# Kernel optimization log

Hardware: AMD Instinct MI355X
Metric: run time of the kernel (lower is better)

## Reference

```python
import jax, jax.numpy as jnp
import numpy as np

B, S = 4, 2048
D_MODEL, N_HEADS, D_KV = 1024, 16, 64
NUM_BUCKETS, MAX_DIST = 32, 128


def _relative_position_bucket(relative_position, num_buckets=NUM_BUCKETS, max_distance=MAX_DIST):
    # bidirectional (encoder) variant, faithful to FlaxT5Attention._relative_position_bucket
    num_buckets = num_buckets // 2
    relative_buckets = (relative_position > 0).astype(jnp.int32) * num_buckets
    rp = jnp.abs(relative_position)
    max_exact = num_buckets // 2
    is_small = rp < max_exact
    rp_large = max_exact + (
        jnp.log(rp.astype(jnp.float32) / max_exact)
        / np.log(max_distance / max_exact)
        * (num_buckets - max_exact)
    )
    rp_large = jnp.minimum(rp_large, num_buckets - 1)
    return relative_buckets + jnp.where(is_small, rp, rp_large.astype(jnp.int32))


def setup_inputs() -> dict:
    key = jax.random.key(0)
    ks = jax.random.split(key, 6)
    return {
        "hidden_states": jax.random.normal(ks[0], (B, S, D_MODEL), jnp.float32),
        "mask": jnp.zeros((B, S), jnp.float32),  # additive mask, 0 = attend
        "wq": jax.random.normal(ks[1], (D_MODEL, N_HEADS * D_KV), jnp.float32) * 0.02,
        "wk": jax.random.normal(ks[2], (D_MODEL, N_HEADS * D_KV), jnp.float32) * 0.02,
        "wv": jax.random.normal(ks[3], (D_MODEL, N_HEADS * D_KV), jnp.float32) * 0.02,
        "wo": jax.random.normal(ks[4], (N_HEADS * D_KV, D_MODEL), jnp.float32) * 0.02,
        "rel_bias": jax.random.normal(ks[5], (NUM_BUCKETS, N_HEADS), jnp.float32) * 0.02,
    }


def reference(hidden_states, mask, wq, wk, wv, wo, rel_bias):
    b, s, _ = hidden_states.shape
    # QKV projections, split heads -> [B, S, H, D]
    q = (hidden_states @ wq).reshape(b, s, N_HEADS, D_KV)
    k = (hidden_states @ wk).reshape(b, s, N_HEADS, D_KV)
    v = (hidden_states @ wv).reshape(b, s, N_HEADS, D_KV)

    # relative position bias -> [1, H, S, S]
    pos = jnp.arange(s, dtype=jnp.int32)
    relative_position = pos[None, :] - pos[:, None]  # memory - query
    buckets = _relative_position_bucket(relative_position)
    position_bias = rel_bias[buckets].transpose(2, 0, 1)[None]  # [1,H,S,S]
    # encoder path: additive mask expanded to [B,1,1,K]
    position_bias = position_bias + mask[:, None, None, :]

    # flax dot_product_attention_weights scales q by 1/sqrt(depth)
    scores = jnp.einsum("bqhd,bkhd->bhqk", q / jnp.sqrt(jnp.float32(D_KV)), k)
    attn_weights = jax.nn.softmax(scores + position_bias, axis=-1)

    attn_output = jnp.einsum("bhqk,bkhd->bqhd", attn_weights, v)
    attn_output = attn_output.reshape(b, s, N_HEADS * D_KV) @ wo
    return attn_output, position_bias
```

## Files before the change

kernel.cpp:

```cpp
#include <hip/hip_runtime.h>
#include <hip/hip_bf16.h>

typedef __attribute__((ext_vector_type(8))) short bf16x8;
typedef __attribute__((ext_vector_type(8))) unsigned short u16x8;
typedef __attribute__((ext_vector_type(4))) float f32x4;

#define B_   4
#define S_   2048
#define H_   16
#define DKV  64
#define DM   1024

static __device__ __forceinline__ f32x4 mfma16(bf16x8 a, bf16x8 b, f32x4 c){
  return __builtin_amdgcn_mfma_f32_16x16x32_bf16(a, b, c, 0, 0, 0);
}
static __device__ __forceinline__ void gload_lds16(const void* g, void* l){
  __builtin_amdgcn_global_load_lds((const __attribute__((address_space(1))) void*)g,
                                   (__attribute__((address_space(3))) void*)l, 16, 0, 0);
}
static __device__ __forceinline__ unsigned short f2b(float f){
  union { __hip_bfloat16 b; unsigned short u; } x;
  x.b = __float2bfloat16(f);
  return x.u;
}

__global__ void cast_h_kernel(const float* __restrict__ in, unsigned short* __restrict__ out, int n4){
  int i = blockIdx.x * 256 + threadIdx.x;
  if (i >= n4) return;
  float4 v = reinterpret_cast<const float4*>(in)[i];
  ushort4 r;
  r.x = f2b(v.x); r.y = f2b(v.y); r.z = f2b(v.z); r.w = f2b(v.w);
  reinterpret_cast<ushort4*>(out)[i] = r;
}

__global__ void transpose_w_kernel(const float* __restrict__ w0, const float* __restrict__ w1,
                                   const float* __restrict__ w2, const float* __restrict__ w3,
                                   unsigned short* o0, unsigned short* o1,
                                   unsigned short* o2, unsigned short* o3){
  int z = blockIdx.z;
  const float* src = (z==0) ? w0 : (z==1) ? w1 : (z==2) ? w2 : w3;
  unsigned short* dst = (z==0) ? o0 : (z==1) ? o1 : (z==2) ? o2 : o3;
  __shared__ float tile[32][33];
  int bx = blockIdx.x * 32, by = blockIdx.y * 32;
  int tx = threadIdx.x, ty = threadIdx.y;
  #pragma unroll
  for (int i = 0; i < 32; i += 8)
    tile[ty + i][tx] = src[(size_t)(by + ty + i) * DM + bx + tx];
  __syncthreads();
  #pragma unroll
  for (int i = 0; i < 32; i += 8)
    dst[(size_t)(bx + ty + i) * DM + by + tx] = f2b(tile[tx][ty + i]);
}

__global__ void build_table_kernel(const float* __restrict__ rel_bias, float* __restrict__ table_t){
  int i = blockIdx.x * 256 + threadIdx.x;
  if (i >= 16 * 4095) return;
  int h = i / 4095;
  int idx = i - h * 4095;
  int rel = idx - 2047;
  int bucket = (rel > 0) ? 16 : 0;
  int rp = (rel < 0) ? -rel : rel;
  int off;
  if (rp < 8) off = rp;
  else off = 8 + (rp>=12) + (rp>=16) + (rp>=23) + (rp>=32) + (rp>=46) + (rp>=64) + (rp>=91);
  table_t[i] = rel_bias[(bucket + off) * 16 + h];
}

__global__ void posbias_kernel(const float* __restrict__ relb, const float* __restrict__ mask,
                               float* __restrict__ out){
  __shared__ float rbh[32];
  int row = blockIdx.x;
  int q = row & (S_ - 1);
  int h = (row >> 11) & (H_ - 1);
  int b = row >> 15;
  int tid = threadIdx.x;
  if (tid < 32) rbh[tid] = relb[tid * 16 + h];
  __syncthreads();
  const float* mrow = mask + b * S_;
  float* orow = out + (size_t)row * S_;
  int k0 = tid * 8;
  #pragma unroll
  for (int c = 0; c < 2; ++c){
    float4 mv = *(const float4*)(mrow + k0 + c * 4);
    float4 v;
    #pragma unroll
    for (int j = 0; j < 4; ++j){
      int k = k0 + c * 4 + j;
      int rel = k - q;
      int bucket = (rel > 0) ? 16 : 0;
      int rp = (rel < 0) ? -rel : rel;
      int off = (rp < 8) ? rp
              : 8 + (rp>=12) + (rp>=16) + (rp>=23) + (rp>=32) + (rp>=46) + (rp>=64) + (rp>=91);
      (&v.x)[j] = rbh[bucket + off] + (&mv.x)[j];
    }
    *(float4*)(orow + k0 + c*4) = v;
  }
}

template<int MODE>
__global__ __launch_bounds__(256, 2) void gemm_bt_kernel(
    const unsigned short* __restrict__ A, const unsigned short* __restrict__ Bt,
    void* __restrict__ outp, int M, int N, int K, float scale)
{
  __shared__ __align__(16) unsigned short As[2][128 * 32];
  __shared__ __align__(16) unsigned short Bs[2][128 * 32];
  int tid = threadIdx.x; int lane = tid & 63; int w = tid >> 6;
  int wr = w >> 1, wc = w & 1;
  int n0 = blockIdx.x * 128, m0 = blockIdx.y * 128;
  const char* Ab = (const char*)A;
  const char* Bb = (const char*)Bt;
  size_t Kb = (size_t)K * 2;

  f32x4 acc[4][4];
  #pragma unroll
  for (int i = 0; i < 4; ++i)
    #pragma unroll
    for (int j = 0; j < 4; ++j) acc[i][j] = (f32x4){0.f, 0.f, 0.f, 0.f};

  auto stage = [&](int kt, int bsel){
    size_t k0b = (size_t)kt * 64;
    #pragma unroll
    for (int c = 0; c < 2; ++c){
      int o = c * 4096 + w * 1024 + lane * 16;
      int row = o >> 6;
      int wbl = (o & 63) ^ (((row >> 1) & 3) << 4);
      gload_lds16(Ab + (size_t)(m0 + row) * Kb + k0b + wbl, (char*)As[bsel] + c * 4096 + w * 1024);
      gload_lds16(Bb + (size_t)(n0 + row) * Kb + k0b + wbl, (char*)Bs[bsel] + c * 4096 + w * 1024);
    }
  };

  int nk = K >> 5;
  int buf = 0;
  stage(0, 0);
  for (int kt = 0; kt < nk; ++kt){
    __syncthreads();
    if (kt + 1 < nk) stage(kt + 1, buf ^ 1);
    bf16x8 af[4], bfr[4];
    #pragma unroll
    for (int f = 0; f < 4; ++f){
      int row = wr * 64 + f * 16 + (lane & 15);
      int byt = (row * 64 + ((lane >> 4) * 16)) ^ (((row >> 1) & 3) << 4);
      af[f] = *(const bf16x8*)((const char*)As[buf] + byt);
    }
    #pragma unroll
    for (int f = 0; f < 4; ++f){
      int row = wc * 64 + f * 16 + (lane & 15);
      int byt = (row * 64 + ((lane >> 4) * 16)) ^ (((row >> 1) & 3) << 4);
      bfr[f] = *(const bf16x8*)((const char*)Bs[buf] + byt);
    }
    #pragma unroll
    for (int i = 0; i < 4; ++i)
      #pragma unroll
      for (int j = 0; j < 4; ++j)
        acc[i][j] = mfma16(af[i], bfr[j], acc[i][j]);
    buf ^= 1;
  }

  #pragma unroll
  for (int i = 0; i < 4; ++i){
    #pragma unroll
    for (int j = 0; j < 4; ++j){
      #pragma unroll
      for (int r = 0; r < 4; ++r){
        int m = m0 + wr * 64 + i * 16 + ((lane >> 4) * 4) + r;
        int n = n0 + wc * 64 + j * 16 + (lane & 15);
        if (MODE == 0){
          ((float*)outp)[(size_t)m * N + n] = acc[i][j][r] * scale;
        } else {
          int sel = n >> 10, nn = n & 1023;
          float v = acc[i][j][r] * (sel == 0 ? 0.125f : 1.0f);
          int b = m >> 11, s = m & 2047, hh = nn >> 6, d = nn & 63;
          ((unsigned short*)outp)[(size_t)sel * 8388608 +
              (((size_t)(b * H_ + hh) * S_) + s) * DKV + d] = f2b(v);
        }
      }
    }
  }
}

__global__ __launch_bounds__(256, 2) void attn_mfma_kernel(
    const unsigned short* __restrict__ Qp, const unsigned short* __restrict__ Kp,
    const unsigned short* __restrict__ Vp, const float* __restrict__ table_t,
    const float* __restrict__ mask, unsigned short* __restrict__ outp)
{
  __shared__ __align__(16) unsigned short Ks[64][72];
  __shared__ __align__(16) unsigned short Vs[64][72];
  __shared__ __align__(16) unsigned short Ps[4][32][72];
  __shared__ float bias_s[191];
  __shared__ float mask_s[64];

  int bid = blockIdx.x;
  int qt = bid & 15; int h = (bid >> 4) & 15; int b = bid >> 8;
  int qb = qt * 128;
  const unsigned short* qptr = Qp + ((size_t)(b * H_ + h) * S_ + qb) * DKV;
  const unsigned short* kptr = Kp + (size_t)(b * H_ + h) * S_ * DKV;
  const unsigned short* vptr = Vp + (size_t)(b * H_ + h) * S_ * DKV;
  int tid = threadIdx.x; int lane = tid & 63; int w = tid >> 6;

  bf16x8 qf[2][2];
  #pragma unroll
  for (int qs = 0; qs < 2; ++qs){
    const unsigned short* qrow = qptr + (size_t)(w * 32 + qs * 16 + (lane & 15)) * DKV + 8 * (lane >> 4);
    qf[qs][0] = *(const bf16x8*)qrow;
    qf[qs][1] = *(const bf16x8*)(qrow + 32);
  }
  float l_r[2][4] = {{0.f,0.f,0.f,0.f},{0.f,0.f,0.f,0.f}};
  f32x4 o_acc[2][4];
  #pragma unroll
  for (int qs = 0; qs < 2; ++qs)
    #pragma unroll
    for (int d = 0; d < 4; ++d) o_acc[qs][d] = (f32x4){0.f, 0.f, 0.f, 0.f};

  int bias_base = h * 4095 + (2047 - qb - 127);

  int skey = tid & 63;
  int sd0  = (tid >> 6) * 16;

  u16x8 ka, kb2, va, vb2;
  float biasr = 0.f, maskr = 0.f;
  auto gload = [&](int k0){
    const unsigned short* krow = kptr + (size_t)(k0 + skey) * DKV + sd0;
    const unsigned short* vrow = vptr + (size_t)(k0 + skey) * DKV + sd0;
    ka  = *(const u16x8*)krow;
    kb2 = *(const u16x8*)(krow + 8);
    va  = *(const u16x8*)vrow;
    vb2 = *(const u16x8*)(vrow + 8);
    if (tid < 191) biasr = table_t[bias_base + k0 + tid];
    else if (tid >= 192) maskr = mask[b * S_ + k0 + (tid - 192)];
  };
  auto lwrite = [&](){
    *(u16x8*)&Ks[skey][sd0]     = ka;
    *(u16x8*)&Ks[skey][sd0 + 8] = kb2;
    #pragma unroll
    for (int j = 0; j < 8; ++j){
      Vs[sd0 + j][skey]     = va[j];
      Vs[sd0 + 8 + j][skey] = vb2[j];
    }
    if (tid < 191) bias_s[tid] = biasr;
    else if (tid >= 192) mask_s[tid - 192] = maskr;
  };

  gload(0);
  lwrite();
  for (int k0 = 0; k0 < S_; k0 += 64){
    __syncthreads();
    if (k0 + 64 < S_) gload(k0 + 64);

    bf16x8 kf[4][2];
    #pragma unroll
    for (int kb = 0; kb < 4; ++kb)
      #pragma unroll
      for (int ks = 0; ks < 2; ++ks)
        kf[kb][ks] = *(const bf16x8*)&Ks[kb * 16 + (lane & 15)][ks * 32 + (lane >> 4) * 8];

    float t[2][4][4];
    float rs[2][4] = {{0.f,0.f,0.f,0.f},{0.f,0.f,0.f,0.f}};
    #pragma unroll
    for (int qs = 0; qs < 2; ++qs){
      f32x4 sc[4];
      #pragma unroll
      for (int kb = 0; kb < 4; ++kb){
        sc[kb] = (f32x4){0.f, 0.f, 0.f, 0.f};
        #pragma unroll
        for (int ks = 0; ks < 2; ++ks)
          sc[kb] = mfma16(qf[qs][ks], kf[kb][ks], sc[kb]);
      }
      #pragma unroll
      for (int kb = 0; kb < 4; ++kb){
        int k_l = kb * 16 + (lane & 15);
        float mk = mask_s[k_l];
        #pragma unroll
        for (int r = 0; r < 4; ++r){
          int q_l = w * 32 + qs * 16 + (lane >> 4) * 4 + r;
          float p = __expf(sc[kb][r] + bias_s[k_l - q_l + 127] + mk);
          t[qs][kb][r] = p;
          rs[qs][r] += p;
        }
      }
    }
    #pragma unroll
    for (int qs = 0; qs < 2; ++qs)
      #pragma unroll
      for (int r = 0; r < 4; ++r){
        #pragma unroll
        for (int off = 1; off < 16; off <<= 1)
          rs[qs][r] += __shfl_xor(rs[qs][r], off, 64);
        l_r[qs][r] += rs[qs][r];
      }
    #pragma unroll
    for (int qs = 0; qs < 2; ++qs)
      #pragma unroll
      for (int kb = 0; kb < 4; ++kb)
        #pragma unroll
        for (int r = 0; r < 4; ++r)
          Ps[w][qs * 16 + (lane >> 4) * 4 + r][kb * 16 + (lane & 15)] = f2b(t[qs][kb][r]);

    bf16x8 vf[4][2];
    #pragma unroll
    for (int db = 0; db < 4; ++db)
      #pragma unroll
      for (int ks = 0; ks < 2; ++ks)
        vf[db][ks] = *(const bf16x8*)&Vs[db * 16 + (lane & 15)][ks * 32 + (lane >> 4) * 8];
    #pragma unroll
    for (int qs = 0; qs < 2; ++qs){
      bf16x8 pa[2];
      #pragma unroll
      for (int ks = 0; ks < 2; ++ks)
        pa[ks] = *(const bf16x8*)&Ps[w][qs * 16 + (lane & 15)][ks * 32 + (lane >> 4) * 8];
      #pragma unroll
      for (int db = 0; db < 4; ++db)
        #pragma unroll
        for (int ks = 0; ks < 2; ++ks)
          o_acc[qs][db] = mfma16(pa[ks], vf[db][ks], o_acc[qs][db]);
    }

    __syncthreads();
    if (k0 + 64 < S_) lwrite();
  }

  #pragma unroll
  for (int qs = 0; qs < 2; ++qs)
    #pragma unroll
    for (int r = 0; r < 4; ++r){
      float inv = 1.0f / l_r[qs][r];
      int qg = qb + w * 32 + qs * 16 + (lane >> 4) * 4 + r;
      size_t rowoff = ((size_t)b * S_ + qg) * DM + h * DKV;
      #pragma unroll
      for (int db = 0; db < 4; ++db)
        outp[rowoff + db * 16 + (lane & 15)] = f2b(o_acc[qs][db][r] * inv);
    }
}

extern "C" void kernel_launch(void* const* d_in, const int* in_sizes, int n_in,
                              void* d_out, int out_size, void* d_ws, size_t ws_size,
                              hipStream_t stream) {
  const float* hs   = (const float*)d_in[0];
  const float* msk  = (const float*)d_in[1];
  const float* wq   = (const float*)d_in[2];
  const float* wk   = (const float*)d_in[3];
  const float* wv   = (const float*)d_in[4];
  const float* wo   = (const float*)d_in[5];
  const float* relb = (const float*)d_in[6];

  float* out_attn = (float*)d_out;
  float* out_pb   = (float*)d_out + (size_t)B_ * S_ * DM;

  const size_t SCRATCH_NEED = 76021760;
  char* ws = (ws_size >= SCRATCH_NEED && d_ws) ? (char*)d_ws : (char*)out_pb;

  unsigned short* h_bf  = (unsigned short*)(ws + 0);
  unsigned short* wqkv_t= (unsigned short*)(ws + 16777216);
  unsigned short* wk_t  = (unsigned short*)(ws + 18874368);
  unsigned short* wv_t  = (unsigned short*)(ws + 20971520);
  unsigned short* wo_t  = (unsigned short*)(ws + 23068672);
  unsigned short* qkv_b = (unsigned short*)(ws + 25165824);
  unsigned short* k_b   = (unsigned short*)(ws + 41943040);
  unsigned short* v_b   = (unsigned short*)(ws + 58720256);
  float*          tabl  = (float*)(ws + 75497472);

  cast_h_kernel<<<8192, 256, 0, stream>>>(hs, h_bf, (B_ * S_ * DM) / 4);
  transpose_w_kernel<<<dim3(32, 32, 4), dim3(32, 8), 0, stream>>>(wq, wk, wv, wo,
                                                                  wqkv_t, wk_t, wv_t, wo_t);
  build_table_kernel<<<256, 256, 0, stream>>>(relb, tabl);

  gemm_bt_kernel<1><<<dim3(24, 64), 256, 0, stream>>>(h_bf, wqkv_t, qkv_b, 8192, 3072, 1024, 1.0f);

  attn_mfma_kernel<<<B_ * H_ * 16, 256, 0, stream>>>(qkv_b, k_b, v_b, tabl, msk, h_bf);

  gemm_bt_kernel<0><<<dim3(8, 64), 256, 0, stream>>>(h_bf, wo_t, out_attn, 8192, 1024, 1024, 1.0f);

  posbias_kernel<<<B_ * H_ * S_, 256, 0, stream>>>(relb, msk, out_pb);
}
```

Before: 484.5 us.

## Double-buffer attention K/V LDS tiles and merge prep kernels into one launch

The attention kernel now keeps two LDS buffers each for K, V, bias and mask, so the next tile is written into the alternate buffer and the second __syncthreads per iteration is dropped. Separately, the cast, weight-transpose and bias-table kernels are merged into one prep kernel to remove two launches. Double buffering raises LDS use per block, which may hurt occupancy at two blocks per CU. The merged prep kernel keeps a __syncthreads inside a block-uniform branch, which is safe.

After: 479.3 us (median of 2 runs). No clear change (-1.1%).

```diff
diff --git a/kernel.cpp b/kernel.cpp
--- a/kernel.cpp
+++ b/kernel.cpp
@@ -24,46 +24,46 @@
   return x.u;
 }
 
-__global__ void cast_h_kernel(const float* __restrict__ in, unsigned short* __restrict__ out, int n4){
-  int i = blockIdx.x * 256 + threadIdx.x;
-  if (i >= n4) return;
-  float4 v = reinterpret_cast<const float4*>(in)[i];
-  ushort4 r;
-  r.x = f2b(v.x); r.y = f2b(v.y); r.z = f2b(v.z); r.w = f2b(v.w);
-  reinterpret_cast<ushort4*>(out)[i] = r;
-}
-
-__global__ void transpose_w_kernel(const float* __restrict__ w0, const float* __restrict__ w1,
-                                   const float* __restrict__ w2, const float* __restrict__ w3,
-                                   unsigned short* o0, unsigned short* o1,
-                                   unsigned short* o2, unsigned short* o3){
-  int z = blockIdx.z;
-  const float* src = (z==0) ? w0 : (z==1) ? w1 : (z==2) ? w2 : w3;
-  unsigned short* dst = (z==0) ? o0 : (z==1) ? o1 : (z==2) ? o2 : o3;
+__global__ void prep_kernel(const float* __restrict__ hs, unsigned short* __restrict__ h_bf,
+                            const float* __restrict__ w0, const float* __restrict__ w1,
+                            const float* __restrict__ w2, const float* __restrict__ w3,
+                            unsigned short* o0, unsigned short* o1,
+                            unsigned short* o2, unsigned short* o3,
+                            const float* __restrict__ rel_bias, float* __restrict__ table_t){
   __shared__ float tile[32][33];
-  int bx = blockIdx.x * 32, by = blockIdx.y * 32;
-  int tx = threadIdx.x, ty = threadIdx.y;
-  #pragma unroll
-  for (int i = 0; i < 32; i += 8)
-    tile[ty + i][tx] = src[(size_t)(by + ty + i) * DM + bx + tx];
-  __syncthreads();
-  #pragma unroll
-  for (int i = 0; i < 32; i += 8)
-    dst[(size_t)(bx + ty + i) * DM + by + tx] = f2b(tile[tx][ty + i]);
-}
-
-__global__ void build_table_kernel(const float* __restrict__ rel_bias, float* __restrict__ table_t){
-  int i = blockIdx.x * 256 + threadIdx.x;
-  if (i >= 16 * 4095) return;
-  int h = i / 4095;
-  int idx = i - h * 4095;
-  int rel = idx - 2047;
-  int bucket = (rel > 0) ? 16 : 0;
-  int rp = (rel < 0) ? -rel : rel;
-  int off;
-  if (rp < 8) off = rp;
-  else off = 8 + (rp>=12) + (rp>=16) + (rp>=23) + (rp>=32) + (rp>=46) + (rp>=64) + (rp>=91);
-  table_t[i] = rel_bias[(bucket + off) * 16 + h];
+  int bid = blockIdx.x, tid = threadIdx.x;
+  if (bid < 8192){
+    int i = bid * 256 + tid;
+    float4 v = reinterpret_cast<const float4*>(hs)[i];
+    ushort4 r;
+    r.x = f2b(v.x); r.y = f2b(v.y); r.z = f2b(v.z); r.w = f2b(v.w);
+    reinterpret_cast<ushort4*>(h_bf)[i] = r;
+  } else if (bid < 12288){
+    int t = bid - 8192;
+    int z = t >> 10, by = (t >> 5) & 31, bx = t & 31;
+    const float* src = (z==0) ? w0 : (z==1) ? w1 : (z==2) ? w2 : w3;
+    unsigned short* dst = (z==0) ? o0 : (z==1) ? o1 : (z==2) ? o2 : o3;
+    int tx = tid & 31, ty = tid >> 5;
+    #pragma unroll
+    for (int i = 0; i < 32; i += 8)
+      tile[ty + i][tx] = src[(size_t)(by * 32 + ty + i) * DM + bx * 32 + tx];
+    __syncthreads();
+    #pragma unroll
+    for (int i = 0; i < 32; i += 8)
+      dst[(size_t)(bx * 32 + ty + i) * DM + by * 32 + tx] = f2b(tile[tx][ty + i]);
+  } else {
+    int i = (bid - 12288) * 256 + tid;
+    if (i < 16 * 4095){
+      int h = i / 4095;
+      int idx = i - h * 4095;
+      int rel = idx - 2047;
+      int bucket = (rel > 0) ? 16 : 0;
+      int rp = (rel < 0) ? -rel : rel;
+      int off = (rp < 8) ? rp
+              : 8 + (rp>=12) + (rp>=16) + (rp>=23) + (rp>=32) + (rp>=46) + (rp>=64) + (rp>=91);
+      table_t[i] = rel_bias[(bucket + off) * 16 + h];
+    }
+  }
 }
 
 __global__ void posbias_kernel(const float* __restrict__ relb, const float* __restrict__ mask,
@@ -183,11 +183,11 @@
     const unsigned short* __restrict__ Vp, const float* __restrict__ table_t,
     const float* __restrict__ mask, unsigned short* __restrict__ outp)
 {
-  __shared__ __align__(16) unsigned short Ks[64][72];
-  __shared__ __align__(16) unsigned short Vs[64][72];
+  __shared__ __align__(16) unsigned short Ks[2][64][72];
+  __shared__ __align__(16) unsigned short Vs[2][64][72];
   __shared__ __align__(16) unsigned short Ps[4][32][72];
-  __shared__ float bias_s[191];
-  __shared__ float mask_s[64];
+  __shared__ float bias_s[2][191];
+  __shared__ float mask_s[2][64];
 
   int bid = blockIdx.x;
   int qt = bid & 15; int h = (bid >> 4) & 15; int b = bid >> 8;
@@ -228,20 +228,21 @@
     if (tid < 191) biasr = table_t[bias_base + k0 + tid];
     else if (tid >= 192) maskr = mask[b * S_ + k0 + (tid - 192)];
   };
-  auto lwrite = [&](){
-    *(u16x8*)&Ks[skey][sd0]     = ka;
-    *(u16x8*)&Ks[skey][sd0 + 8] = kb2;
+  auto lwrite = [&](int bsel){
+    *(u16x8*)&Ks[bsel][skey][sd0]     = ka;
+    *(u16x8*)&Ks[bsel][skey][sd0 + 8] = kb2;
     #pragma unroll
     for (int j = 0; j < 8; ++j){
-      Vs[sd0 + j][skey]     = va[j];
-      Vs[sd0 + 8 + j][skey] = vb2[j];
-    }
-    if (tid < 191) bias_s[tid] = biasr;
-    else if (tid >= 192) mask_s[tid - 192] = maskr;
+      Vs[bsel][sd0 + j][skey]     = va[j];
+      Vs[bsel][sd0 + 8 + j][skey] = vb2[j];
+    }
+    if (tid < 191) bias_s[bsel][tid] = biasr;
+    else if (tid >= 192) mask_s[bsel][tid - 192] = maskr;
   };
 
   gload(0);
-  lwrite();
+  lwrite(0);
+  int cur = 0;
   for (int k0 = 0; k0 < S_; k0 += 64){
     __syncthreads();
     if (k0 + 64 < S_) gload(k0 + 64);
@@ -251,7 +252,7 @@
     for (int kb = 0; kb < 4; ++kb)
       #pragma unroll
       for (int ks = 0; ks < 2; ++ks)
-        kf[kb][ks] = *(const bf16x8*)&Ks[kb * 16 + (lane & 15)][ks * 32 + (lane >> 4) * 8];
+        kf[kb][ks] = *(const bf16x8*)&Ks[cur][kb * 16 + (lane & 15)][ks * 32 + (lane >> 4) * 8];
 
     float t[2][4][4];
     float rs[2][4] = {{0.f,0.f,0.f,0.f},{0.f,0.f,0.f,0.f}};
@@ -268,11 +269,11 @@
       #pragma unroll
       for (int kb = 0; kb < 4; ++kb){
         int k_l = kb * 16 + (lane & 15);
-        float mk = mask_s[k_l];
+        float mk = mask_s[cur][k_l];
         #pragma unroll
         for (int r = 0; r < 4; ++r){
           int q_l = w * 32 + qs * 16 + (lane >> 4) * 4 + r;
-          float p = __expf(sc[kb][r] + bias_s[k_l - q_l + 127] + mk);
+          float p = __expf(sc[kb][r] + bias_s[cur][k_l - q_l + 127] + mk);
           t[qs][kb][r] = p;
           rs[qs][r] += p;
         }
@@ -300,7 +301,7 @@
     for (int db = 0; db < 4; ++db)
       #pragma unroll
       for (int ks = 0; ks < 2; ++ks)
-        vf[db][ks] = *(const bf16x8*)&Vs[db * 16 + (lane & 15)][ks * 32 + (lane >> 4) * 8];
+        vf[db][ks] = *(const bf16x8*)&Vs[cur][db * 16 + (lane & 15)][ks * 32 + (lane >> 4) * 8];
     #pragma unroll
     for (int qs = 0; qs < 2; ++qs){
       bf16x8 pa[2];
@@ -314,8 +315,8 @@
           o_acc[qs][db] = mfma16(pa[ks], vf[db][ks], o_acc[qs][db]);
     }
 
-    __syncthreads();
-    if (k0 + 64 < S_) lwrite();
+    if (k0 + 64 < S_) lwrite(cur ^ 1);
+    cur ^= 1;
   }
 
   #pragma unroll
@@ -358,10 +359,8 @@
   unsigned short* v_b   = (unsigned short*)(ws + 58720256);
   float*          tabl  = (float*)(ws + 75497472);
 
-  cast_h_kernel<<<8192, 256, 0, stream>>>(hs, h_bf, (B_ * S_ * DM) / 4);
-  transpose_w_kernel<<<dim3(32, 32, 4), dim3(32, 8), 0, stream>>>(wq, wk, wv, wo,
-                                                                  wqkv_t, wk_t, wv_t, wo_t);
-  build_table_kernel<<<256, 256, 0, stream>>>(relb, tabl);
+  prep_kernel<<<12544, 256, 0, stream>>>(hs, h_bf, wq, wk, wv, wo,
+                                         wqkv_t, wk_t, wv_t, wo_t, relb, tabl);
 
   gemm_bt_kernel<1><<<dim3(24, 64), 256, 0, stream>>>(h_bf, wqkv_t, qkv_b, 8192, 3072, 1024, 1.0f);
 
```
